# Performance work log

Hardware: AMD Instinct MI355X
Metric: run time of the kernel (lower is better)

## Reference

```python
import jax, jax.numpy as jnp
import numpy as np

LAMBDA1 = 0.3366
LAMBDA2 = 0.2424
LAMBDA3 = 0.06
LR = 0.1
N_ITERS = 10          # fixed iteration count standing in for the eps-based while loop
BETA1, BETA2, ADAM_EPS = 0.9, 0.999, 1e-8


def setup_inputs() -> dict:
    key = jax.random.key(0)
    k1, k2, k3 = jax.random.split(key, 3)
    D, T, K = 512, 50000, 16
    return {
        "embedding": jax.random.normal(k1, (D, T), jnp.float32),
        "basis_init": jax.random.normal(k2, (D, K), jnp.float32),
        "activation_init": jax.random.normal(k3, (K, T), jnp.float32),
        "k": K,
    }


def _matrix_l1(X):
    # torch.linalg.norm(X, ord=1) on a 2D tensor = induced 1-norm = max column abs-sum
    return jnp.max(jnp.sum(jnp.abs(X), axis=0))


def _jitter(A):
    # temporal jitter penalty: sum of abs frame-to-frame differences
    return jnp.sum(jnp.abs(A[:, 1:] - A[:, :-1]))


def _shrink(X):
    # faithful to the (buggy) torch _shrink: sign(X) * max(0, |X - lr*l|)
    return jnp.sign(X) * jnp.maximum(0.0, jnp.abs(X - LR * LAMBDA1))


def _adam(p, g, m, v, t):
    m = BETA1 * m + (1.0 - BETA1) * g
    v = BETA2 * v + (1.0 - BETA2) * g * g
    mh = m / (1.0 - BETA1 ** t)
    vh = v / (1.0 - BETA2 ** t)
    p = p - LR * mh / (jnp.sqrt(vh) + ADAM_EPS)
    return p, m, v


def _run(embedding, basis_init, activation_init):
    A = activation_init  # optimizer_act.step() is never called in the source -> A is constant

    def loss_from_B(B):
        return (_matrix_l1(embedding - B @ A)
                + LAMBDA1 * _matrix_l1(B)
                + LAMBDA2 * _matrix_l1(A)
                + LAMBDA3 * _jitter(A))

    # iteration 1: loss is computed on the raw parameter (shrink applied after the step)
    P = basis_init
    m = jnp.zeros_like(P)
    v = jnp.zeros_like(P)
    g = jax.grad(loss_from_B)(P)
    P, m, v = _adam(P, g, m, v, jnp.float32(1.0))

    # iterations 2..N: loss sees shrink(P); gradient flows through the shrink into P
    def step(carry, t):
        P, m, v = carry
        g = jax.grad(lambda p: loss_from_B(_shrink(p)))(P)
        P, m, v = _adam(P, g, m, v, t)
        return (P, m, v), None

    ts = jnp.arange(2, N_ITERS + 1, dtype=jnp.float32)
    (P, m, v), _ = jax.lax.scan(step, (P, m, v), ts)
    return _shrink(P), A


def reference(embedding, basis_init, activation_init, k):
    # returns (embedding_basis_matrix, activation_matrix) as in OutputDiarization
    return _run(embedding, basis_init, activation_init)
```

## Files before the change

kernel.cpp:

```cpp
#include <hip/hip_runtime.h>
#include <hip/hip_cooperative_groups.h>

namespace cg = cooperative_groups;

#define D 512
#define T 50000
#define K 16
#define NIT 10

#define NBLK 256
#define BTH  512
#define COLS_PER_BLOCK 196
#define NGRP 49
#define PASSES 2

#define NLEAF 16
#define BLK_PER_LEAF (NBLK / NLEAF)
#define BAR_PAD 32

#define LAMBDA1 0.3366f
#define LR      0.1f
#define SHRINK_C (LR * LAMBDA1)
#define BETA1   0.9f
#define BETA2   0.999f
#define ADAM_EPS 1e-8f

__device__ __forceinline__ float sgn(float x) {
    return (x > 0.f) ? 1.f : ((x < 0.f) ? -1.f : 0.f);
}

__device__ __forceinline__ void accum_row(const float4 e, const float* __restrict__ brow,
                                          const float4* __restrict__ a4, float4& acc) {
    float bb[K];
    *reinterpret_cast<float4*>(&bb[0])  = reinterpret_cast<const float4*>(brow)[0];
    *reinterpret_cast<float4*>(&bb[4])  = reinterpret_cast<const float4*>(brow)[1];
    *reinterpret_cast<float4*>(&bb[8])  = reinterpret_cast<const float4*>(brow)[2];
    *reinterpret_cast<float4*>(&bb[12]) = reinterpret_cast<const float4*>(brow)[3];
    float4 r = e;
#pragma unroll
    for (int k = 0; k < K; ++k) {
        r.x = fmaf(-bb[k], a4[k].x, r.x);
        r.y = fmaf(-bb[k], a4[k].y, r.y);
        r.z = fmaf(-bb[k], a4[k].z, r.z);
        r.w = fmaf(-bb[k], a4[k].w, r.w);
    }
    acc.x += fabsf(r.x); acc.y += fabsf(r.y);
    acc.z += fabsf(r.z); acc.w += fabsf(r.w);
}

__device__ __forceinline__ void bar_arrive_wait(unsigned long long* __restrict__ bar,
                                                int it0, int bid) {
    unsigned long long* leaf = &bar[(size_t)((it0 * NLEAF) + (bid & (NLEAF - 1))) * BAR_PAD];
    unsigned long long* root = &bar[(size_t)((NIT * NLEAF) + it0) * BAR_PAD];
    __threadfence();
    if (atomicAdd(leaf, 1ull) == (unsigned long long)(BLK_PER_LEAF - 1)) {
        __threadfence();
        atomicAdd(root, 1ull);
    }
    long long guard = 0;
    while (__hip_atomic_load(root, __ATOMIC_RELAXED, __HIP_MEMORY_SCOPE_AGENT)
           < (unsigned long long)NLEAF) {
        __builtin_amdgcn_s_sleep(2);
        if (++guard > (1ll << 26)) break;
    }
    __threadfence();
}

__global__ __launch_bounds__(BTH, 2) void diar_all(
        const float* __restrict__ E, const float* __restrict__ Bin,
        const float* __restrict__ A, float* __restrict__ out,
        unsigned long long* __restrict__ slot, unsigned long long* __restrict__ bar) {
    __shared__ __align__(16) float Bl[D * K];
    __shared__ float4 psum[16][32];
    __shared__ float wsum[8][K];
    __shared__ float colA[K];
    __shared__ int js_s, ks_s;

    const int tid = threadIdx.x;
    const int bid = blockIdx.x;
    cg::grid_group grid = cg::this_grid();

    float pr[K], mr[K], vr[K];
    {
        const float4* src = reinterpret_cast<const float4*>(Bin + tid * K);
        float4* bl4 = reinterpret_cast<float4*>(&Bl[tid * K]);
#pragma unroll
        for (int q = 0; q < 4; ++q) {
            float4 x = src[q];
            bl4[q] = x;
            pr[4 * q + 0] = x.x; pr[4 * q + 1] = x.y;
            pr[4 * q + 2] = x.z; pr[4 * q + 3] = x.w;
        }
#pragma unroll
        for (int k = 0; k < K; ++k) { mr[k] = 0.f; vr[k] = 0.f; }
    }
    if (bid == 0) {
        const int nbar = (NIT * NLEAF + NIT) * BAR_PAD;
        for (int q = tid; q < nbar; q += BTH) bar[q] = 0ull;
        if (tid < NIT) slot[tid] = 0ull;
        __threadfence();
    }
    __syncthreads();
    grid.sync();

    const int c = tid & 31;
    const int s = tid >> 5;

    float b1p = 1.f, b2p = 1.f;

    for (int it = 1; it <= NIT; ++it) {
        b1p *= BETA1; b2p *= BETA2;

        unsigned long long key = 0ull;
#pragma unroll
        for (int p = 0; p < PASSES; ++p) {
            const int g = p * 32 + c;
            const int j0 = bid * COLS_PER_BLOCK + g * 4;
            const bool ok = (g < NGRP) && (j0 < T);
            float4 acc = {0.f, 0.f, 0.f, 0.f};
            if (ok) {
                float4 a4[K];
#pragma unroll
                for (int k = 0; k < K; ++k)
                    a4[k] = *reinterpret_cast<const float4*>(A + (size_t)k * T + j0);
                const int rbase = s * 32;
                const float* Ep = E + j0;
                float4 eb[8];
#pragma unroll
                for (int ch = 0; ch < 4; ++ch) {
#pragma unroll
                    for (int u = 0; u < 8; ++u)
                        eb[u] = *reinterpret_cast<const float4*>(
                            Ep + (size_t)(rbase + ch * 8 + u) * T);
#pragma unroll
                    for (int u = 0; u < 8; ++u)
                        accum_row(eb[u], &Bl[(rbase + ch * 8 + u) * K], a4, acc);
                }
            }
            psum[s][c] = acc;
            __syncthreads();
            if (tid < 32) {
                const int gg = p * 32 + tid;
                const int jb = bid * COLS_PER_BLOCK + gg * 4;
                if (gg < NGRP && jb < T) {
                    float4 cs = psum[0][tid];
#pragma unroll
                    for (int q = 1; q < 16; ++q) {
                        float4 pq = psum[q][tid];
                        cs.x += pq.x; cs.y += pq.y; cs.z += pq.z; cs.w += pq.w;
                    }
                    float v4[4] = {cs.x, cs.y, cs.z, cs.w};
#pragma unroll
                    for (int q = 0; q < 4; ++q) {
                        unsigned long long kq =
                            (((unsigned long long)__float_as_uint(v4[q])) << 32)
                            | (unsigned int)(jb + q);
                        if (kq > key) key = kq;
                    }
                }
            }
            __syncthreads();
        }
        if (tid < 64) {
#pragma unroll
            for (int off = 32; off > 0; off >>= 1) {
                unsigned long long o = __shfl_down(key, off, 64);
                if (o > key) key = o;
            }
            if (tid == 0) atomicMax(&slot[it - 1], key);
        }

        if (tid == 0) {
            bar_arrive_wait(bar, it - 1, bid);
            unsigned long long kk = atomicMax(&slot[it - 1], 0ull);
            js_s = (int)(kk & 0xffffffffull);
        }
        __syncthreads();
        const int js = js_s;
        if (tid < K) colA[tid] = A[(size_t)tid * T + js];

        float cb[K];
        {
            const float* brow = &Bl[tid * K];
#pragma unroll
            for (int k = 0; k < K; ++k) cb[k] = fabsf(brow[k]);
#pragma unroll
            for (int off = 32; off > 0; off >>= 1) {
#pragma unroll
                for (int k = 0; k < K; ++k) cb[k] += __shfl_down(cb[k], off, 64);
            }
            if ((tid & 63) == 0) {
                const int w = tid >> 6;
#pragma unroll
                for (int k = 0; k < K; ++k) wsum[w][k] = cb[k];
            }
        }
        __syncthreads();
        if (tid == 0) {
            float best = -1.f; int kb = 0;
#pragma unroll
            for (int k = 0; k < K; ++k) {
                float t = 0.f;
                for (int w = 0; w < 8; ++w) t += wsum[w][k];
                if (t > best) { best = t; kb = k; }
            }
            ks_s = kb;
        }
        __syncthreads();
        const int ks = ks_s;
        const float biasm = 1.f - b1p;
        const float biasv = 1.f - b2p;

        float r = E[(size_t)tid * T + js];
        const float* brow = &Bl[tid * K];
#pragma unroll
        for (int k = 0; k < K; ++k) r = fmaf(-brow[k], colA[k], r);
        const float sg = sgn(r);

#pragma unroll
        for (int k = 0; k < K; ++k) {
            float g = -sg * colA[k];
            if (k == ks) g += LAMBDA1 * sgn(brow[k]);
            float p = pr[k];
            if (it >= 2) g *= sgn(p) * sgn(p - SHRINK_C);
            float mm = BETA1 * mr[k] + (1.f - BETA1) * g;
            float vv = BETA2 * vr[k] + (1.f - BETA2) * g * g;
            mr[k] = mm; vr[k] = vv;
            p -= LR * (mm / biasm) / (sqrtf(vv / biasv) + ADAM_EPS);
            pr[k] = p;
        }
        {
            float4* bl4 = reinterpret_cast<float4*>(&Bl[tid * K]);
#pragma unroll
            for (int q = 0; q < 4; ++q) {
                float4 x;
                x.x = sgn(pr[4 * q + 0]) * fmaxf(0.f, fabsf(pr[4 * q + 0] - SHRINK_C));
                x.y = sgn(pr[4 * q + 1]) * fmaxf(0.f, fabsf(pr[4 * q + 1] - SHRINK_C));
                x.z = sgn(pr[4 * q + 2]) * fmaxf(0.f, fabsf(pr[4 * q + 2] - SHRINK_C));
                x.w = sgn(pr[4 * q + 3]) * fmaxf(0.f, fabsf(pr[4 * q + 3] - SHRINK_C));
                bl4[q] = x;
            }
        }
        __syncthreads();
    }

    if (bid == 0) {
        float4* o4 = reinterpret_cast<float4*>(out);
        const float4* b4 = reinterpret_cast<const float4*>(Bl);
#pragma unroll
        for (int q = 0; q < 4; ++q) o4[tid * 4 + q] = b4[tid * 4 + q];
    }
    {
        float4* o4 = reinterpret_cast<float4*>(out) + (D * K) / 4;
        const float4* a4p = reinterpret_cast<const float4*>(A);
        const int n4 = (K * T) / 4;
        for (int q = bid * BTH + tid; q < n4; q += NBLK * BTH) o4[q] = a4p[q];
    }
}

extern "C" void kernel_launch(void* const* d_in, const int* in_sizes, int n_in,
                              void* d_out, int out_size, void* d_ws, size_t ws_size,
                              hipStream_t stream) {
    const float* E   = (const float*)d_in[0];
    const float* Bin = (const float*)d_in[1];
    const float* A   = (const float*)d_in[2];
    float* out = (float*)d_out;
    unsigned long long* slot = (unsigned long long*)d_ws;
    unsigned long long* bar  = (unsigned long long*)((char*)d_ws + 1024);

    void* args[] = { (void*)&E, (void*)&Bin, (void*)&A, (void*)&out,
                     (void*)&slot, (void*)&bar };
    hipLaunchCooperativeKernel((void*)diar_all, dim3(NBLK), dim3(BTH),
                               args, 0, stream);
}
```

Baseline: 878.2 us.

## Double block size to 1024 threads with two columns per thread

Doubles threads per block and switches each thread from four columns (float4) to two columns (float2), so each block covers its column range with more wavefronts. Block-level reduction buffers and guards are resized, and the per-row Adam update is limited to the first 512 threads. The aim is more memory-level parallelism and latency hiding in the streaming residual pass. In exchange, loads become narrower, the launch bound no longer requests two blocks per CU, and the threads beyond row 512 sit idle during the update phase.

```diff
diff --git a/kernel.cpp b/kernel.cpp
--- a/kernel.cpp
+++ b/kernel.cpp
@@ -9,9 +9,9 @@
 #define NIT 10
 
 #define NBLK 256
-#define BTH  512
+#define BTH  1024
 #define COLS_PER_BLOCK 196
-#define NGRP 49
+#define GRP2 98
 #define PASSES 2
 
 #define NLEAF 16
@@ -29,23 +29,20 @@
     return (x > 0.f) ? 1.f : ((x < 0.f) ? -1.f : 0.f);
 }
 
-__device__ __forceinline__ void accum_row(const float4 e, const float* __restrict__ brow,
-                                          const float4* __restrict__ a4, float4& acc) {
+__device__ __forceinline__ void accum_row2(const float2 e, const float* __restrict__ brow,
+                                           const float2* __restrict__ a2, float2& acc) {
     float bb[K];
     *reinterpret_cast<float4*>(&bb[0])  = reinterpret_cast<const float4*>(brow)[0];
     *reinterpret_cast<float4*>(&bb[4])  = reinterpret_cast<const float4*>(brow)[1];
     *reinterpret_cast<float4*>(&bb[8])  = reinterpret_cast<const float4*>(brow)[2];
     *reinterpret_cast<float4*>(&bb[12]) = reinterpret_cast<const float4*>(brow)[3];
-    float4 r = e;
+    float2 r = e;
 #pragma unroll
     for (int k = 0; k < K; ++k) {
-        r.x = fmaf(-bb[k], a4[k].x, r.x);
-        r.y = fmaf(-bb[k], a4[k].y, r.y);
-        r.z = fmaf(-bb[k], a4[k].z, r.z);
-        r.w = fmaf(-bb[k], a4[k].w, r.w);
+        r.x = fmaf(-bb[k], a2[k].x, r.x);
+        r.y = fmaf(-bb[k], a2[k].y, r.y);
     }
     acc.x += fabsf(r.x); acc.y += fabsf(r.y);
-    acc.z += fabsf(r.z); acc.w += fabsf(r.w);
 }
 
 __device__ __forceinline__ void bar_arrive_wait(unsigned long long* __restrict__ bar,
@@ -66,12 +63,12 @@
     __threadfence();
 }
 
-__global__ __launch_bounds__(BTH, 2) void diar_all(
+__global__ __launch_bounds__(BTH) void diar_all(
         const float* __restrict__ E, const float* __restrict__ Bin,
         const float* __restrict__ A, float* __restrict__ out,
         unsigned long long* __restrict__ slot, unsigned long long* __restrict__ bar) {
     __shared__ __align__(16) float Bl[D * K];
-    __shared__ float4 psum[16][32];
+    __shared__ float2 psum[16][64];
     __shared__ float wsum[8][K];
     __shared__ float colA[K];
     __shared__ int js_s, ks_s;
@@ -81,7 +78,7 @@
     cg::grid_group grid = cg::this_grid();
 
     float pr[K], mr[K], vr[K];
-    {
+    if (tid < D) {
         const float4* src = reinterpret_cast<const float4*>(Bin + tid * K);
         float4* bl4 = reinterpret_cast<float4*>(&Bl[tid * K]);
 #pragma unroll
@@ -103,8 +100,8 @@
     __syncthreads();
     grid.sync();
 
-    const int c = tid & 31;
-    const int s = tid >> 5;
+    const int c = tid & 63;
+    const int s = tid >> 6;
 
     float b1p = 1.f, b2p = 1.f;
 
@@ -114,46 +111,46 @@
         unsigned long long key = 0ull;
 #pragma unroll
         for (int p = 0; p < PASSES; ++p) {
-            const int g = p * 32 + c;
-            const int j0 = bid * COLS_PER_BLOCK + g * 4;
-            const bool ok = (g < NGRP) && (j0 < T);
-            float4 acc = {0.f, 0.f, 0.f, 0.f};
+            const int g = p * 64 + c;
+            const int j0 = bid * COLS_PER_BLOCK + g * 2;
+            const bool ok = (g < GRP2);
+            float2 acc = {0.f, 0.f};
             if (ok) {
-                float4 a4[K];
+                float2 a2[K];
 #pragma unroll
                 for (int k = 0; k < K; ++k)
-                    a4[k] = *reinterpret_cast<const float4*>(A + (size_t)k * T + j0);
+                    a2[k] = *reinterpret_cast<const float2*>(A + (size_t)k * T + j0);
                 const int rbase = s * 32;
                 const float* Ep = E + j0;
-                float4 eb[8];
-#pragma unroll
-                for (int ch = 0; ch < 4; ++ch) {
-#pragma unroll
-                    for (int u = 0; u < 8; ++u)
-                        eb[u] = *reinterpret_cast<const float4*>(
-                            Ep + (size_t)(rbase + ch * 8 + u) * T);
-#pragma unroll
-                    for (int u = 0; u < 8; ++u)
-                        accum_row(eb[u], &Bl[(rbase + ch * 8 + u) * K], a4, acc);
+                float2 eb[4];
+#pragma unroll
+                for (int ch = 0; ch < 8; ++ch) {
+#pragma unroll
+                    for (int u = 0; u < 4; ++u)
+                        eb[u] = *reinterpret_cast<const float2*>(
+                            Ep + (size_t)(rbase + ch * 4 + u) * T);
+#pragma unroll
+                    for (int u = 0; u < 4; ++u)
+                        accum_row2(eb[u], &Bl[(rbase + ch * 4 + u) * K], a2, acc);
                 }
             }
             psum[s][c] = acc;
             __syncthreads();
-            if (tid < 32) {
-                const int gg = p * 32 + tid;
-                const int jb = bid * COLS_PER_BLOCK + gg * 4;
-                if (gg < NGRP && jb < T) {
-                    float4 cs = psum[0][tid];
+            if (tid < 64) {
+                const int gg = p * 64 + tid;
+                if (gg < GRP2) {
+                    float2 cs = psum[0][tid];
 #pragma unroll
                     for (int q = 1; q < 16; ++q) {
-                        float4 pq = psum[q][tid];
-                        cs.x += pq.x; cs.y += pq.y; cs.z += pq.z; cs.w += pq.w;
+                        float2 pq = psum[q][tid];
+                        cs.x += pq.x; cs.y += pq.y;
                     }
-                    float v4[4] = {cs.x, cs.y, cs.z, cs.w};
-#pragma unroll
-                    for (int q = 0; q < 4; ++q) {
+                    const int jb = bid * COLS_PER_BLOCK + gg * 2;
+                    float v2[2] = {cs.x, cs.y};
+#pragma unroll
+                    for (int q = 0; q < 2; ++q) {
                         unsigned long long kq =
-                            (((unsigned long long)__float_as_uint(v4[q])) << 32)
+                            (((unsigned long long)__float_as_uint(v2[q])) << 32)
                             | (unsigned int)(jb + q);
                         if (kq > key) key = kq;
                     }
@@ -179,9 +176,9 @@
         const int js = js_s;
         if (tid < K) colA[tid] = A[(size_t)tid * T + js];
 
-        float cb[K];
-        {
+        if (tid < D) {
             const float* brow = &Bl[tid * K];
+            float cb[K];
 #pragma unroll
             for (int k = 0; k < K; ++k) cb[k] = fabsf(brow[k]);
 #pragma unroll
@@ -211,25 +208,25 @@
         const float biasm = 1.f - b1p;
         const float biasv = 1.f - b2p;
 
-        float r = E[(size_t)tid * T + js];
-        const float* brow = &Bl[tid * K];
-#pragma unroll
-        for (int k = 0; k < K; ++k) r = fmaf(-brow[k], colA[k], r);
-        const float sg = sgn(r);
-
-#pragma unroll
-        for (int k = 0; k < K; ++k) {
-            float g = -sg * colA[k];
-            if (k == ks) g += LAMBDA1 * sgn(brow[k]);
-            float p = pr[k];
-            if (it >= 2) g *= sgn(p) * sgn(p - SHRINK_C);
-            float mm = BETA1 * mr[k] + (1.f - BETA1) * g;
-            float vv = BETA2 * vr[k] + (1.f - BETA2) * g * g;
-            mr[k] = mm; vr[k] = vv;
-            p -= LR * (mm / biasm) / (sqrtf(vv / biasv) + ADAM_EPS);
-            pr[k] = p;
-        }
-        {
+        if (tid < D) {
+            float r = E[(size_t)tid * T + js];
+            const float* brow = &Bl[tid * K];
+#pragma unroll
+            for (int k = 0; k < K; ++k) r = fmaf(-brow[k], colA[k], r);
+            const float sg = sgn(r);
+
+#pragma unroll
+            for (int k = 0; k < K; ++k) {
+                float g = -sg * colA[k];
+                if (k == ks) g += LAMBDA1 * sgn(brow[k]);
+                float p = pr[k];
+                if (it >= 2) g *= sgn(p) * sgn(p - SHRINK_C);
+                float mm = BETA1 * mr[k] + (1.f - BETA1) * g;
+                float vv = BETA2 * vr[k] + (1.f - BETA2) * g * g;
+                mr[k] = mm; vr[k] = vv;
+                p -= LR * (mm / biasm) / (sqrtf(vv / biasv) + ADAM_EPS);
+                pr[k] = p;
+            }
             float4* bl4 = reinterpret_cast<float4*>(&Bl[tid * K]);
 #pragma unroll
             for (int q = 0; q < 4; ++q) {
@@ -244,7 +241,7 @@
         __syncthreads();
     }
 
-    if (bid == 0) {
+    if (bid == 0 && tid < D) {
         float4* o4 = reinterpret_cast<float4*>(out);
         const float4* b4 = reinterpret_cast<const float4*>(Bl);
 #pragma unroll
```

New measurement: 1.691 ms. 92.5% more time.
